# Kernel optimization log

Hardware: AMD Instinct MI355X
Metric: run time of the kernel (lower is better)

## Reference

```python
import jax, jax.numpy as jnp
import numpy as np

B, T, D = 4, 2048, 2048
H = 16
NOPE, ROPE, VD = 64, 64, 128
QK = NOPE + ROPE  # 128
KV_R, Q_R = 512, 1024
EPS = 1e-6
THETA = 10000.0
SCALE = 1.0 / np.sqrt(QK)


def rmsnorm(x, g):
    var = jnp.mean(jnp.square(x), axis=-1, keepdims=True)
    return x * jax.lax.rsqrt(var + EPS) * g


def rope_tables(seq_len, dim):
    inv_freq = 1.0 / (THETA ** (np.arange(0, dim, 2, dtype=np.float32) / dim))
    t = np.arange(seq_len, dtype=np.float32)
    freqs = np.outer(t, inv_freq)              # [T, dim/2]
    emb = np.concatenate([freqs, freqs], -1)   # [T, dim]
    return jnp.asarray(np.cos(emb)), jnp.asarray(np.sin(emb))


def rotate_half(x):
    x1, x2 = jnp.split(x, 2, axis=-1)
    return jnp.concatenate([-x2, x1], axis=-1)


def apply_rope(x, cos, sin):
    # x: [B,H,S,dim]; cos/sin: [S,dim] -> broadcast over B,H
    return x * cos[None, None] + rotate_half(x) * sin[None, None]


def setup_inputs() -> dict:
    key = jax.random.key(0)
    ks = jax.random.split(key, 10)
    w = lambda k, shp: jax.random.normal(k, shp, jnp.float32) * 0.02
    return {
        'x': jax.random.normal(ks[0], (B, T, D), jnp.float32),
        'w_q_down': w(ks[1], (D, Q_R)),
        'g_q_down': jnp.ones((Q_R,), jnp.float32),
        'w_q_up': w(ks[2], (Q_R, H * QK)),
        'w_kv_down': w(ks[3], (D, KV_R)),
        'g_kv_down': jnp.ones((KV_R,), jnp.float32),
        'w_k_up': w(ks[4], (KV_R, H * NOPE)),
        'w_v_up': w(ks[5], (KV_R, H * VD)),
        'w_k_rope': w(ks[6], (D, ROPE)),
        'g_q': jnp.ones((QK,), jnp.float32),
        'g_k': jnp.ones((QK,), jnp.float32),
        'w_gate': w(ks[7], (D, H * VD)),
        'w_o': w(ks[8], (H * VD, D)),
    }


def reference(x, w_q_down, g_q_down, w_q_up, w_kv_down, g_kv_down,
              w_k_up, w_v_up, w_k_rope, g_q, g_k, w_gate, w_o):
    cos, sin = rope_tables(T, ROPE)

    # Low-rank Q: down-proj -> RMSNorm -> up-proj
    q_c = rmsnorm(x @ w_q_down, g_q_down)                       # [B,T,Q_R]
    q = (q_c @ w_q_up).reshape(B, T, H, QK).transpose(0, 2, 1, 3)  # [B,H,T,QK]
    q_nope, q_rope = q[..., :NOPE], q[..., NOPE:]

    # Low-rank KV compression
    c_kv = rmsnorm(x @ w_kv_down, g_kv_down)                    # [B,S,KV_R]
    k_rope = x @ w_k_rope                                       # [B,S,ROPE]
    S = T
    k_nope = (c_kv @ w_k_up).reshape(B, S, H, NOPE).transpose(0, 2, 1, 3)
    v = (c_kv @ w_v_up).reshape(B, S, H, VD).transpose(0, 2, 1, 3)

    # Decoupled RoPE: shared k_rope broadcast over heads
    k_rope = jnp.broadcast_to(k_rope[:, None], (B, H, S, ROPE))
    q_rope = apply_rope(q_rope, cos[:T], sin[:T])
    k_rope = apply_rope(k_rope, cos[:S], sin[:S])

    q = rmsnorm(jnp.concatenate([q_nope, q_rope], -1), g_q)     # [B,H,T,QK]
    k = rmsnorm(jnp.concatenate([k_nope, k_rope], -1), g_k)     # [B,H,S,QK]

    # Causal SDPA
    scores = jnp.einsum('bhtd,bhsd->bhts', q, k) * SCALE
    mask = jnp.tril(jnp.ones((T, S), bool))
    scores = jnp.where(mask, scores, jnp.finfo(scores.dtype).min)
    attn = jax.nn.softmax(scores, axis=-1)
    out = jnp.einsum('bhts,bhsd->bhtd', attn, v)                # [B,H,T,VD]

    # Gating
    gate = (x @ w_gate).reshape(B, T, H, VD).transpose(0, 2, 1, 3)
    out = out * jax.nn.silu(gate)

    out = out.transpose(0, 2, 1, 3).reshape(B, T, H * VD)
    return out @ w_o
```

## Files before the change

### kernel.cpp

```cpp
#include <hip/hip_runtime.h>
#include <hip/hip_bf16.h>
#include <math.h>

typedef __bf16 bf16_t;
typedef __bf16 bf16x4 __attribute__((ext_vector_type(4)));
typedef __bf16 bf16x8 __attribute__((ext_vector_type(8)));
typedef float f32x4 __attribute__((ext_vector_type(4)));

#define SCALE_F 0.08838834764831845f
#define SMAX_F 14.0f

#define GLOAD_LDS16(gp, lp)                                              \
    __builtin_amdgcn_global_load_lds(                                    \
        (const __attribute__((address_space(1))) void*)(gp),             \
        (__attribute__((address_space(3))) void*)(lp), 16, 0, 0)

__global__ void k_convert(const float* __restrict__ in, bf16_t* __restrict__ out, int n) {
    int i = (blockIdx.x * 256 + threadIdx.x) * 4;
    if (i >= n) return;
    float4 f = *(const float4*)(in + i);
    out[i + 0] = (bf16_t)f.x;
    out[i + 1] = (bf16_t)f.y;
    out[i + 2] = (bf16_t)f.z;
    out[i + 3] = (bf16_t)f.w;
}

__global__ void k_transpose(const float* __restrict__ w, bf16_t* __restrict__ wt, int K, int N) {
    __shared__ float tile[32][33];
    int n0 = blockIdx.x * 32, k0 = blockIdx.y * 32;
    int tx = threadIdx.x & 31, ty = threadIdx.x >> 5;
#pragma unroll
    for (int i = 0; i < 32; i += 8)
        tile[ty + i][tx] = w[(size_t)(k0 + ty + i) * N + (n0 + tx)];
    __syncthreads();
#pragma unroll
    for (int i = 0; i < 32; i += 8)
        wt[(size_t)(n0 + ty + i) * K + (k0 + tx)] = (bf16_t)tile[tx][ty + i];
}

__global__ void k_rope_tables(float* __restrict__ cosT, float* __restrict__ sinT) {
    int idx = blockIdx.x * 256 + threadIdx.x;
    int t = idx >> 6, i = idx & 63;
    float invf = powf(10000.f, -(float)(i & 31) / 32.f);
    float ang = (float)t * invf;
    float s, c;
    sincosf(ang, &s, &c);
    cosT[idx] = c;
    sinT[idx] = s;
}

__global__ void k_rmsnorm(bf16_t* __restrict__ x, const float* __restrict__ g, int C) {
    bf16_t* p = x + (size_t)blockIdx.x * C;
    float ss = 0.f;
    for (int i = threadIdx.x; i < C; i += 256) {
        float v = (float)p[i];
        ss += v * v;
    }
#pragma unroll
    for (int m = 32; m; m >>= 1) ss += __shfl_xor(ss, m);
    __shared__ float red[4];
    if ((threadIdx.x & 63) == 0) red[threadIdx.x >> 6] = ss;
    __syncthreads();
    float tot = red[0] + red[1] + red[2] + red[3];
    float scale = rsqrtf(tot / (float)C + 1e-6f);
    for (int i = threadIdx.x; i < C; i += 256)
        p[i] = (bf16_t)((float)p[i] * scale * g[i]);
}

template <int OUTF32>
__global__ __launch_bounds__(256) void k_gemm(const bf16_t* __restrict__ A,
                                              const bf16_t* __restrict__ Bt,
                                              void* __restrict__ Cp, int M, int N, int K,
                                              size_t sA, size_t sB, size_t sC) {
    __shared__ bf16_t As[2][128 * 32];
    __shared__ bf16_t Bs[2][128 * 32];
    A += (size_t)blockIdx.z * sA;
    Bt += (size_t)blockIdx.z * sB;
    const size_t coff = (size_t)blockIdx.z * sC;
    const int bm = blockIdx.y * 128, bn = blockIdx.x * 128;
    const int tid = threadIdx.x, lane = tid & 63, wv = tid >> 6;
    const int quad = lane >> 4, l16 = lane & 15;
    const int wm = (wv >> 1) * 64, wn = (wv & 1) * 64;
    f32x4 acc[4][4] = {};
    const int sr0 = wv * 32 + (lane >> 2);
    const int scc = (lane & 3) * 8;
    const int lo0 = (wv * 2) * 512, lo1 = (wv * 2 + 1) * 512;
    const bool bok0 = (bn + sr0) < N;
    const bool bok1 = (bn + sr0 + 16) < N;
    for (int k0 = 0; k0 < K; k0 += 64) {
        const bf16_t* gA = A + (size_t)(bm + sr0) * K + k0 + scc;
        const bf16_t* gB = Bt + (size_t)(bn + sr0) * K + k0 + scc;
        GLOAD_LDS16(gA, As[0] + lo0);
        GLOAD_LDS16(gA + (size_t)16 * K, As[0] + lo1);
        GLOAD_LDS16(gA + 32, As[1] + lo0);
        GLOAD_LDS16(gA + (size_t)16 * K + 32, As[1] + lo1);
        if (bok0) {
            GLOAD_LDS16(gB, Bs[0] + lo0);
            GLOAD_LDS16(gB + 32, Bs[1] + lo0);
        }
        if (bok1) {
            GLOAD_LDS16(gB + (size_t)16 * K, Bs[0] + lo1);
            GLOAD_LDS16(gB + (size_t)16 * K + 32, Bs[1] + lo1);
        }
        __syncthreads();
#pragma unroll
        for (int hf = 0; hf < 2; ++hf) {
            bf16x8 af[4], bfr[4];
#pragma unroll
            for (int mi = 0; mi < 4; ++mi)
                af[mi] = *(bf16x8*)(As[hf] + (wm + mi * 16 + l16) * 32 + quad * 8);
#pragma unroll
            for (int ni = 0; ni < 4; ++ni)
                bfr[ni] = *(bf16x8*)(Bs[hf] + (wn + ni * 16 + l16) * 32 + quad * 8);
#pragma unroll
            for (int mi = 0; mi < 4; ++mi)
#pragma unroll
                for (int ni = 0; ni < 4; ++ni)
                    acc[mi][ni] = __builtin_amdgcn_mfma_f32_16x16x32_bf16(af[mi], bfr[ni],
                                                                          acc[mi][ni], 0, 0, 0);
        }
        __syncthreads();
    }
#pragma unroll
    for (int mi = 0; mi < 4; ++mi)
#pragma unroll
        for (int ni = 0; ni < 4; ++ni)
#pragma unroll
            for (int r = 0; r < 4; ++r) {
                int row = bm + wm + mi * 16 + quad * 4 + r;
                int col = bn + wn + ni * 16 + l16;
                if (col < N) {
                    if constexpr (OUTF32)
                        ((float*)Cp)[coff + (size_t)row * N + col] = acc[mi][ni][r];
                    else
                        ((bf16_t*)Cp)[coff + (size_t)row * N + col] = (bf16_t)acc[mi][ni][r];
                }
            }
}

__global__ void k_build_q(bf16_t* __restrict__ q, const float* __restrict__ g,
                          const float* __restrict__ cosT, const float* __restrict__ sinT) {
    int wid = blockIdx.x * 4 + (threadIdx.x >> 6);
    int lane = threadIdx.x & 63;
    int row = wid >> 4, h = wid & 15;
    int t = row & 2047;
    bf16_t* p = q + (size_t)row * 2048 + h * 128;
    float x0 = (float)p[lane];
    float x1 = (float)p[64 + lane];
    float xp = (float)p[64 + (lane ^ 32)];
    float c = cosT[t * 64 + lane], s = sinT[t * 64 + lane];
    float rot = (lane < 32) ? -xp : xp;
    float y1 = x1 * c + rot * s;
    float ss = x0 * x0 + y1 * y1;
#pragma unroll
    for (int m = 32; m; m >>= 1) ss += __shfl_xor(ss, m);
    float scale = rsqrtf(ss / 128.f + 1e-6f);
    p[lane] = (bf16_t)(x0 * scale * g[lane]);
    p[64 + lane] = (bf16_t)(y1 * scale * g[64 + lane]);
}

__global__ void k_build_k(const bf16_t* __restrict__ knope, const bf16_t* __restrict__ krope,
                          bf16_t* __restrict__ kout, const float* __restrict__ g,
                          const float* __restrict__ cosT, const float* __restrict__ sinT) {
    int wid = blockIdx.x * 4 + (threadIdx.x >> 6);
    int lane = threadIdx.x & 63;
    int row = wid >> 4, h = wid & 15;
    int t = row & 2047;
    float x0 = (float)knope[(size_t)row * 1024 + h * 64 + lane];
    float x1 = (float)krope[(size_t)row * 64 + lane];
    float xp = (float)krope[(size_t)row * 64 + (lane ^ 32)];
    float c = cosT[t * 64 + lane], s = sinT[t * 64 + lane];
    float rot = (lane < 32) ? -xp : xp;
    float y1 = x1 * c + rot * s;
    float ss = x0 * x0 + y1 * y1;
#pragma unroll
    for (int m = 32; m; m >>= 1) ss += __shfl_xor(ss, m);
    float scale = rsqrtf(ss / 128.f + 1e-6f);
    bf16_t* p = kout + (size_t)row * 2048 + h * 128;
    p[lane] = (bf16_t)(x0 * scale * g[lane]);
    p[64 + lane] = (bf16_t)(y1 * scale * g[64 + lane]);
}

__global__ __launch_bounds__(256, 2) void k_attn(const bf16_t* __restrict__ q,
                                                 const bf16_t* __restrict__ k,
                                                 const bf16_t* __restrict__ vT,
                                                 const bf16_t* __restrict__ gate,
                                                 bf16_t* __restrict__ o) {
    __shared__ bf16_t Ks[64 * 136];
    __shared__ bf16_t Vt[128 * 72];
    __shared__ float lbuf[128];
    const int qb = (int)gridDim.x - 1 - (int)blockIdx.x;
    const int bh = blockIdx.y;
    const int b = bh >> 4, h = bh & 15;
    const int t0 = qb * 128;
    const int tid = threadIdx.x, lane = tid & 63, wv = tid >> 6;
    const int quad = lane >> 4, l16 = lane & 15;
    const int wrow = t0 + wv * 32;

    bf16x8 aq[2][4];
#pragma unroll
    for (int mi = 0; mi < 2; ++mi) {
        const bf16_t* qp =
            q + ((size_t)(b * 2048 + wrow + mi * 16 + l16)) * 2048 + h * 128 + quad * 8;
#pragma unroll
        for (int kk = 0; kk < 4; ++kk) aq[mi][kk] = *(const bf16x8*)(qp + kk * 32);
    }
    f32x4 oacc[2][8] = {};
    float l_lane[2] = {0.f, 0.f};

    const bf16_t* vbase = vT + ((size_t)b * 2048 + (size_t)h * 128) * 2048;
    const bf16_t* kbase = k + ((size_t)b * 2048) * 2048 + h * 128;

    const int krow = tid >> 4;
    const int kcol = (tid & 15) * 8;
    const int kds = krow * 136 + kcol;
    const int vrow = tid >> 1;
    const int vkk = tid & 1;
    const int vds = vrow * 72 + vkk * 32;

    const int nkb = 2 * qb + 2;
    bf16x8 kreg[4], vreg[4];
    {
#pragma unroll
        for (int i = 0; i < 4; ++i)
            kreg[i] = *(const bf16x8*)(kbase + (size_t)(krow + 16 * i) * 2048 + kcol);
#pragma unroll
        for (int j = 0; j < 4; ++j)
            vreg[j] = *(const bf16x8*)(vbase + (size_t)vrow * 2048 + vkk * 32 + j * 8);
    }
    for (int kb = 0; kb < nkb; ++kb) {
        const int s0 = kb * 64;
        __syncthreads();
#pragma unroll
        for (int i = 0; i < 4; ++i) *(bf16x8*)(Ks + kds + i * (16 * 136)) = kreg[i];
        {
            bf16x8 o0 = __builtin_shufflevector(vreg[0], vreg[2], 0, 1, 2, 3, 8, 9, 10, 11);
            bf16x8 o1 = __builtin_shufflevector(vreg[0], vreg[2], 4, 5, 6, 7, 12, 13, 14, 15);
            bf16x8 o2 = __builtin_shufflevector(vreg[1], vreg[3], 0, 1, 2, 3, 8, 9, 10, 11);
            bf16x8 o3 = __builtin_shufflevector(vreg[1], vreg[3], 4, 5, 6, 7, 12, 13, 14, 15);
            *(bf16x8*)(Vt + vds) = o0;
            *(bf16x8*)(Vt + vds + 8) = o1;
            *(bf16x8*)(Vt + vds + 16) = o2;
            *(bf16x8*)(Vt + vds + 24) = o3;
        }
        __syncthreads();
        if (kb + 1 < nkb) {
            const int sn = s0 + 64;
#pragma unroll
            for (int i = 0; i < 4; ++i)
                kreg[i] = *(const bf16x8*)(kbase + (size_t)(sn + krow + 16 * i) * 2048 + kcol);
#pragma unroll
            for (int j = 0; j < 4; ++j)
                vreg[j] = *(const bf16x8*)(vbase + (size_t)vrow * 2048 + sn + vkk * 32 + j * 8);
        }
        if (s0 > wrow + 31) continue;
        const int tq0 = wrow + l16;
        const int tq1 = wrow + 16 + l16;
        bf16x8 pa[2][2];
#pragma unroll
        for (int ni = 0; ni < 4; ++ni) {
            f32x4 sc0 = {0.f, 0.f, 0.f, 0.f};
            f32x4 sc1 = {0.f, 0.f, 0.f, 0.f};
#pragma unroll
            for (int kk = 0; kk < 4; ++kk) {
                bf16x8 ak = *(bf16x8*)(Ks + (ni * 16 + l16) * 136 + kk * 32 + quad * 8);
                sc0 = __builtin_amdgcn_mfma_f32_16x16x32_bf16(ak, aq[0][kk], sc0, 0, 0, 0);
                sc1 = __builtin_amdgcn_mfma_f32_16x16x32_bf16(ak, aq[1][kk], sc1, 0, 0, 0);
            }
            const int sb = s0 + ni * 16 + quad * 4;
#pragma unroll
            for (int r2 = 0; r2 < 4; ++r2) {
                float pv0 = __expf(sc0[r2] * SCALE_F - SMAX_F);
                float pv1 = __expf(sc1[r2] * SCALE_F - SMAX_F);
                if (sb + r2 > tq0) pv0 = 0.f;
                if (sb + r2 > tq1) pv1 = 0.f;
                l_lane[0] += pv0;
                l_lane[1] += pv1;
                pa[0][ni >> 1][(ni & 1) * 4 + r2] = (bf16_t)pv0;
                pa[1][ni >> 1][(ni & 1) * 4 + r2] = (bf16_t)pv1;
            }
        }
#pragma unroll
        for (int kh = 0; kh < 2; ++kh)
#pragma unroll
            for (int nd = 0; nd < 8; ++nd) {
                bf16x8 bv = *(bf16x8*)(Vt + (nd * 16 + l16) * 72 + kh * 32 + quad * 8);
                oacc[0][nd] =
                    __builtin_amdgcn_mfma_f32_16x16x32_bf16(pa[0][kh], bv, oacc[0][nd], 0, 0, 0);
                oacc[1][nd] =
                    __builtin_amdgcn_mfma_f32_16x16x32_bf16(pa[1][kh], bv, oacc[1][nd], 0, 0, 0);
            }
    }
#pragma unroll
    for (int mi = 0; mi < 2; ++mi) {
        l_lane[mi] += __shfl_xor(l_lane[mi], 16);
        l_lane[mi] += __shfl_xor(l_lane[mi], 32);
    }
    if (quad == 0) {
        lbuf[wv * 32 + l16] = l_lane[0];
        lbuf[wv * 32 + 16 + l16] = l_lane[1];
    }
    float rl[2][4];
#pragma unroll
    for (int mi = 0; mi < 2; ++mi)
#pragma unroll
        for (int r2 = 0; r2 < 4; ++r2)
            rl[mi][r2] = 1.f / lbuf[wv * 32 + mi * 16 + quad * 4 + r2];
#pragma unroll
    for (int mi = 0; mi < 2; ++mi)
#pragma unroll
        for (int nd = 0; nd < 8; ++nd) {
            int d = nd * 16 + l16;
#pragma unroll
            for (int r2 = 0; r2 < 4; ++r2) {
                int trow = wrow + mi * 16 + quad * 4 + r2;
                size_t gi = ((size_t)(b * 2048 + trow)) * 2048 + h * 128 + d;
                float gt = (float)gate[gi];
                float sg = gt / (1.f + __expf(-gt));
                o[gi] = (bf16_t)((oacc[mi][nd][r2] * rl[mi][r2]) * sg);
            }
        }
}

extern "C" void kernel_launch(void* const* d_in, const int* in_sizes, int n_in,
                              void* d_out, int out_size, void* d_ws, size_t ws_size,
                              hipStream_t stream) {
    const float* x         = (const float*)d_in[0];
    const float* w_q_down  = (const float*)d_in[1];
    const float* g_q_down  = (const float*)d_in[2];
    const float* w_q_up    = (const float*)d_in[3];
    const float* w_kv_down = (const float*)d_in[4];
    const float* g_kv_down = (const float*)d_in[5];
    const float* w_k_up    = (const float*)d_in[6];
    const float* w_v_up    = (const float*)d_in[7];
    const float* w_k_rope  = (const float*)d_in[8];
    const float* g_q       = (const float*)d_in[9];
    const float* g_k       = (const float*)d_in[10];
    const float* w_gate    = (const float*)d_in[11];
    const float* w_o       = (const float*)d_in[12];
    float* out = (float*)d_out;

    char* base = (char*)d_ws;
    size_t off = 0;
    auto alloc = [&](size_t bytes) -> void* {
        void* p = base + off;
        off = (off + bytes + 255) & ~(size_t)255;
        return p;
    };
    const size_t MT = 8192;
    bf16_t* xb     = (bf16_t*)alloc(MT * 2048 * 2);
    bf16_t* wqd_t  = (bf16_t*)alloc((size_t)1024 * 2048 * 2);
    bf16_t* wqu_t  = (bf16_t*)alloc((size_t)2048 * 1024 * 2);
    bf16_t* wkvd_t = (bf16_t*)alloc((size_t)512 * 2048 * 2);
    bf16_t* wku_t  = (bf16_t*)alloc((size_t)1024 * 512 * 2);
    bf16_t* wvu_t  = (bf16_t*)alloc((size_t)2048 * 512 * 2);
    bf16_t* wkr_t  = (bf16_t*)alloc((size_t)64 * 2048 * 2);
    bf16_t* wg_t   = (bf16_t*)alloc((size_t)2048 * 2048 * 2);
    bf16_t* wo_t   = (bf16_t*)alloc((size_t)2048 * 2048 * 2);
    bf16_t* qc     = (bf16_t*)alloc(MT * 1024 * 2);
    bf16_t* ckv    = (bf16_t*)alloc(MT * 512 * 2);
    bf16_t* krope  = (bf16_t*)alloc(MT * 64 * 2);
    bf16_t* vT     = (bf16_t*)alloc(MT * 2048 * 2);
    bf16_t* gbuf   = (bf16_t*)alloc(MT * 2048 * 2);
    float* cosT    = (float*)alloc((size_t)2048 * 64 * 4);
    float* sinT    = (float*)alloc((size_t)2048 * 64 * 4);
    bf16_t* knope = qc;
    bf16_t* qbuf  = (bf16_t*)d_out;
    bf16_t* kbuf  = (bf16_t*)d_out + MT * 2048;
    bf16_t* obuf  = xb;

    k_convert<<<dim3(16384), dim3(256), 0, stream>>>(x, xb, 16777216);
    k_transpose<<<dim3(32, 64), 256, 0, stream>>>(w_q_down, wqd_t, 2048, 1024);
    k_transpose<<<dim3(64, 32), 256, 0, stream>>>(w_q_up, wqu_t, 1024, 2048);
    k_transpose<<<dim3(16, 64), 256, 0, stream>>>(w_kv_down, wkvd_t, 2048, 512);
    k_transpose<<<dim3(32, 16), 256, 0, stream>>>(w_k_up, wku_t, 512, 1024);
    k_transpose<<<dim3(64, 16), 256, 0, stream>>>(w_v_up, wvu_t, 512, 2048);
    k_transpose<<<dim3(2, 64), 256, 0, stream>>>(w_k_rope, wkr_t, 2048, 64);
    k_transpose<<<dim3(64, 64), 256, 0, stream>>>(w_gate, wg_t, 2048, 2048);
    k_transpose<<<dim3(64, 64), 256, 0, stream>>>(w_o, wo_t, 2048, 2048);
    k_rope_tables<<<dim3(512), 256, 0, stream>>>(cosT, sinT);
    k_gemm<0><<<dim3(8, 64), 256, 0, stream>>>(xb, wqd_t, qc, 8192, 1024, 2048, 0, 0, 0);
    k_rmsnorm<<<dim3(8192), 256, 0, stream>>>(qc, g_q_down, 1024);
    k_gemm<0><<<dim3(16, 64), 256, 0, stream>>>(qc, wqu_t, qbuf, 8192, 2048, 1024, 0, 0, 0);
    k_gemm<0><<<dim3(4, 64), 256, 0, stream>>>(xb, wkvd_t, ckv, 8192, 512, 2048, 0, 0, 0);
    k_rmsnorm<<<dim3(8192), 256, 0, stream>>>(ckv, g_kv_down, 512);
    k_gemm<0><<<dim3(8, 64), 256, 0, stream>>>(ckv, wku_t, knope, 8192, 1024, 512, 0, 0, 0);
    k_gemm<0><<<dim3(16, 16, 4), 256, 0, stream>>>(wvu_t, ckv, vT, 2048, 2048, 512,
                                                   0, (size_t)2048 * 512, (size_t)2048 * 2048);
    k_gemm<0><<<dim3(1, 64), 256, 0, stream>>>(xb, wkr_t, krope, 8192, 64, 2048, 0, 0, 0);
    k_gemm<0><<<dim3(16, 64), 256, 0, stream>>>(xb, wg_t, gbuf, 8192, 2048, 2048, 0, 0, 0);
    k_build_q<<<dim3(32768), 256, 0, stream>>>(qbuf, g_q, cosT, sinT);
    k_build_k<<<dim3(32768), 256, 0, stream>>>(knope, krope, kbuf, g_k, cosT, sinT);
    k_attn<<<dim3(16, 64), 256, 0, stream>>>(qbuf, kbuf, vT, gbuf, obuf);
    k_gemm<1><<<dim3(16, 64), 256, 0, stream>>>(obuf, wo_t, out, 8192, 2048, 2048, 0, 0, 0);
}
```

Baseline: 793.1 us.

## Double-buffer K/V tiles in LDS and remap attention blocks across XCDs

The attention kernel now keeps two LDS buffers for the K and V^T tiles. The next tile is staged while the current one is consumed, so each iteration needs one barrier instead of two. Block indices are remapped so that all query blocks of a (batch, head) pair land on the same XCD, which is meant to improve L2 reuse of K/V, and the longest query blocks are still scheduled first. The causal mask check is also skipped for key tiles that lie fully below the diagonal. LDS use roughly doubles, which may reduce occupancy at 2 blocks per CU.

New measurement: 705.4 us. 1.12x faster.

```diff
diff --git a/kernel.cpp b/kernel.cpp
--- a/kernel.cpp
+++ b/kernel.cpp
@@ -186,11 +186,13 @@
                                                  const bf16_t* __restrict__ vT,
                                                  const bf16_t* __restrict__ gate,
                                                  bf16_t* __restrict__ o) {
-    __shared__ bf16_t Ks[64 * 136];
-    __shared__ bf16_t Vt[128 * 72];
+    __shared__ bf16_t Ks[2][64 * 136];
+    __shared__ bf16_t Vt[2][128 * 72];
     __shared__ float lbuf[128];
-    const int qb = (int)gridDim.x - 1 - (int)blockIdx.x;
-    const int bh = blockIdx.y;
+    const int lin = (int)blockIdx.x + 16 * (int)blockIdx.y;
+    const int xcd = lin & 7, idx = lin >> 3;
+    const int bh = xcd * 8 + (idx & 7);
+    const int qb = 15 - (idx >> 3);
     const int b = bh >> 4, h = bh & 15;
     const int t0 = qb * 128;
     const int tid = threadIdx.x, lane = tid & 63, wv = tid >> 6;
@@ -220,76 +222,92 @@
 
     const int nkb = 2 * qb + 2;
     bf16x8 kreg[4], vreg[4];
-    {
+    auto LOADREGS = [&](int sn) {
 #pragma unroll
         for (int i = 0; i < 4; ++i)
-            kreg[i] = *(const bf16x8*)(kbase + (size_t)(krow + 16 * i) * 2048 + kcol);
+            kreg[i] = *(const bf16x8*)(kbase + (size_t)(sn + krow + 16 * i) * 2048 + kcol);
 #pragma unroll
         for (int j = 0; j < 4; ++j)
-            vreg[j] = *(const bf16x8*)(vbase + (size_t)vrow * 2048 + vkk * 32 + j * 8);
-    }
+            vreg[j] = *(const bf16x8*)(vbase + (size_t)vrow * 2048 + sn + vkk * 32 + j * 8);
+    };
+    auto STAGE = [&](int buf) {
+#pragma unroll
+        for (int i = 0; i < 4; ++i) *(bf16x8*)(Ks[buf] + kds + i * (16 * 136)) = kreg[i];
+        bf16x8 o0 = __builtin_shufflevector(vreg[0], vreg[2], 0, 1, 2, 3, 8, 9, 10, 11);
+        bf16x8 o1 = __builtin_shufflevector(vreg[0], vreg[2], 4, 5, 6, 7, 12, 13, 14, 15);
+        bf16x8 o2 = __builtin_shufflevector(vreg[1], vreg[3], 0, 1, 2, 3, 8, 9, 10, 11);
+        bf16x8 o3 = __builtin_shufflevector(vreg[1], vreg[3], 4, 5, 6, 7, 12, 13, 14, 15);
+        *(bf16x8*)(Vt[buf] + vds) = o0;
+        *(bf16x8*)(Vt[buf] + vds + 8) = o1;
+        *(bf16x8*)(Vt[buf] + vds + 16) = o2;
+        *(bf16x8*)(Vt[buf] + vds + 24) = o3;
+    };
+    LOADREGS(0);
+    STAGE(0);
+    LOADREGS(64);
+    __syncthreads();
+
     for (int kb = 0; kb < nkb; ++kb) {
         const int s0 = kb * 64;
+        const int cur = kb & 1;
+        if (kb + 1 < nkb) {
+            STAGE(cur ^ 1);
+            if (kb + 2 < nkb) LOADREGS((kb + 2) * 64);
+        }
+        if (s0 <= wrow + 31) {
+            const bf16_t* ksp = Ks[cur];
+            const bf16_t* vtp = Vt[cur];
+            const int tq0 = wrow + l16;
+            const int tq1 = wrow + 16 + l16;
+            const bool dgw = (s0 + 63 > wrow);
+            bf16x8 pa[2][2];
+#pragma unroll
+            for (int ni = 0; ni < 4; ++ni) {
+                f32x4 sc0 = {0.f, 0.f, 0.f, 0.f};
+                f32x4 sc1 = {0.f, 0.f, 0.f, 0.f};
+#pragma unroll
+                for (int kk = 0; kk < 4; ++kk) {
+                    bf16x8 ak = *(bf16x8*)(ksp + (ni * 16 + l16) * 136 + kk * 32 + quad * 8);
+                    sc0 = __builtin_amdgcn_mfma_f32_16x16x32_bf16(ak, aq[0][kk], sc0, 0, 0, 0);
+                    sc1 = __builtin_amdgcn_mfma_f32_16x16x32_bf16(ak, aq[1][kk], sc1, 0, 0, 0);
+                }
+                const int sb = s0 + ni * 16 + quad * 4;
+                if (dgw) {
+#pragma unroll
+                    for (int r2 = 0; r2 < 4; ++r2) {
+                        float pv0 = __expf(sc0[r2] * SCALE_F - SMAX_F);
+                        float pv1 = __expf(sc1[r2] * SCALE_F - SMAX_F);
+                        if (sb + r2 > tq0) pv0 = 0.f;
+                        if (sb + r2 > tq1) pv1 = 0.f;
+                        l_lane[0] += pv0;
+                        l_lane[1] += pv1;
+                        pa[0][ni >> 1][(ni & 1) * 4 + r2] = (bf16_t)pv0;
+                        pa[1][ni >> 1][(ni & 1) * 4 + r2] = (bf16_t)pv1;
+                    }
+                } else {
+#pragma unroll
+                    for (int r2 = 0; r2 < 4; ++r2) {
+                        float pv0 = __expf(sc0[r2] * SCALE_F - SMAX_F);
+                        float pv1 = __expf(sc1[r2] * SCALE_F - SMAX_F);
+                        l_lane[0] += pv0;
+                        l_lane[1] += pv1;
+                        pa[0][ni >> 1][(ni & 1) * 4 + r2] = (bf16_t)pv0;
+                        pa[1][ni >> 1][(ni & 1) * 4 + r2] = (bf16_t)pv1;
+                    }
+                }
+            }
+#pragma unroll
+            for (int kh = 0; kh < 2; ++kh)
+#pragma unroll
+                for (int nd = 0; nd < 8; ++nd) {
+                    bf16x8 bv = *(bf16x8*)(vtp + (nd * 16 + l16) * 72 + kh * 32 + quad * 8);
+                    oacc[0][nd] = __builtin_amdgcn_mfma_f32_16x16x32_bf16(pa[0][kh], bv,
+                                                                          oacc[0][nd], 0, 0, 0);
+                    oacc[1][nd] = __builtin_amdgcn_mfma_f32_16x16x32_bf16(pa[1][kh], bv,
+                                                                          oacc[1][nd], 0, 0, 0);
+                }
+        }
         __syncthreads();
-#pragma unroll
-        for (int i = 0; i < 4; ++i) *(bf16x8*)(Ks + kds + i * (16 * 136)) = kreg[i];
-        {
-            bf16x8 o0 = __builtin_shufflevector(vreg[0], vreg[2], 0, 1, 2, 3, 8, 9, 10, 11);
-            bf16x8 o1 = __builtin_shufflevector(vreg[0], vreg[2], 4, 5, 6, 7, 12, 13, 14, 15);
-            bf16x8 o2 = __builtin_shufflevector(vreg[1], vreg[3], 0, 1, 2, 3, 8, 9, 10, 11);
-            bf16x8 o3 = __builtin_shufflevector(vreg[1], vreg[3], 4, 5, 6, 7, 12, 13, 14, 15);
-            *(bf16x8*)(Vt + vds) = o0;
-            *(bf16x8*)(Vt + vds + 8) = o1;
-            *(bf16x8*)(Vt + vds + 16) = o2;
-            *(bf16x8*)(Vt + vds + 24) = o3;
-        }
-        __syncthreads();
-        if (kb + 1 < nkb) {
-            const int sn = s0 + 64;
-#pragma unroll
-            for (int i = 0; i < 4; ++i)
-                kreg[i] = *(const bf16x8*)(kbase + (size_t)(sn + krow + 16 * i) * 2048 + kcol);
-#pragma unroll
-            for (int j = 0; j < 4; ++j)
-                vreg[j] = *(const bf16x8*)(vbase + (size_t)vrow * 2048 + sn + vkk * 32 + j * 8);
-        }
-        if (s0 > wrow + 31) continue;
-        const int tq0 = wrow + l16;
-        const int tq1 = wrow + 16 + l16;
-        bf16x8 pa[2][2];
-#pragma unroll
-        for (int ni = 0; ni < 4; ++ni) {
-            f32x4 sc0 = {0.f, 0.f, 0.f, 0.f};
-            f32x4 sc1 = {0.f, 0.f, 0.f, 0.f};
-#pragma unroll
-            for (int kk = 0; kk < 4; ++kk) {
-                bf16x8 ak = *(bf16x8*)(Ks + (ni * 16 + l16) * 136 + kk * 32 + quad * 8);
-                sc0 = __builtin_amdgcn_mfma_f32_16x16x32_bf16(ak, aq[0][kk], sc0, 0, 0, 0);
-                sc1 = __builtin_amdgcn_mfma_f32_16x16x32_bf16(ak, aq[1][kk], sc1, 0, 0, 0);
-            }
-            const int sb = s0 + ni * 16 + quad * 4;
-#pragma unroll
-            for (int r2 = 0; r2 < 4; ++r2) {
-                float pv0 = __expf(sc0[r2] * SCALE_F - SMAX_F);
-                float pv1 = __expf(sc1[r2] * SCALE_F - SMAX_F);
-                if (sb + r2 > tq0) pv0 = 0.f;
-                if (sb + r2 > tq1) pv1 = 0.f;
-                l_lane[0] += pv0;
-                l_lane[1] += pv1;
-                pa[0][ni >> 1][(ni & 1) * 4 + r2] = (bf16_t)pv0;
-                pa[1][ni >> 1][(ni & 1) * 4 + r2] = (bf16_t)pv1;
-            }
-        }
-#pragma unroll
-        for (int kh = 0; kh < 2; ++kh)
-#pragma unroll
-            for (int nd = 0; nd < 8; ++nd) {
-                bf16x8 bv = *(bf16x8*)(Vt + (nd * 16 + l16) * 72 + kh * 32 + quad * 8);
-                oacc[0][nd] =
-                    __builtin_amdgcn_mfma_f32_16x16x32_bf16(pa[0][kh], bv, oacc[0][nd], 0, 0, 0);
-                oacc[1][nd] =
-                    __builtin_amdgcn_mfma_f32_16x16x32_bf16(pa[1][kh], bv, oacc[1][nd], 0, 0, 0);
-            }
     }
 #pragma unroll
     for (int mi = 0; mi < 2; ++mi) {
```
